# Optimization experiments

Hardware: AMD Instinct MI355X
Metric: run time of the kernel (lower is better)

## Reference

```python
import jax, jax.numpy as jnp
import numpy as np

B, S, D, H = 4, 2048, 1024, 16
HD = D // H

def setup_inputs() -> dict:
    key = jax.random.key(0)
    ks = jax.random.split(key, 5)
    x = jax.random.normal(ks[0], (B, S, D), dtype=jnp.float32)
    mask = jnp.ones((B, S), dtype=jnp.int32)
    # torch nn.Linear init scale ~ 1/sqrt(fan_in); use small normal for stability
    qkv_w = jax.random.normal(ks[1], (3 * D, D), dtype=jnp.float32) * (1.0 / np.sqrt(D))
    qkv_b = jax.random.normal(ks[2], (3 * D,), dtype=jnp.float32) * 0.02
    out_w = jax.random.normal(ks[3], (D, D), dtype=jnp.float32) * (1.0 / np.sqrt(D))
    out_b = jax.random.normal(ks[4], (D,), dtype=jnp.float32) * 0.02
    return {"x": x, "mask": mask, "qkv_w": qkv_w, "qkv_b": qkv_b,
            "out_w": out_w, "out_b": out_b}

def reference(x, mask, qkv_w, qkv_b, out_w, out_b):
    b, s, d = x.shape
    scale = np.sqrt(HD).astype(np.float32)
    # qkv projection: torch Linear y = x @ W^T + b
    qkv = x @ qkv_w.T + qkv_b                      # (b, s, 3d)
    qkv = qkv.reshape(b, s, 3, H, HD)
    qkv = jnp.transpose(qkv, (2, 0, 3, 1, 4))      # (3, b, H, s, hd)
    q, k, v = qkv[0], qkv[1], qkv[2]
    scores = jnp.einsum('bhqd,bhkd->bhqk', q, k) / scale  # (b, H, s, s)
    neg_inf = jnp.float32(-jnp.inf)
    causal = jnp.tril(jnp.ones((s, s), dtype=bool))
    scores = jnp.where(causal[None, None], scores, neg_inf)
    key_mask = (mask != 0)[:, None, None, :]       # (b, 1, 1, s)
    scores = jnp.where(key_mask, scores, neg_inf)
    attn = jax.nn.softmax(scores, axis=-1)
    out = jnp.einsum('bhqk,bhkd->bhqd', attn, v)   # (b, H, s, hd)
    out = jnp.transpose(out, (0, 2, 1, 3)).reshape(b, s, d)
    return out @ out_w.T + out_b
```

## Files before the change

kernel.cpp:

```cpp
#include <hip/hip_runtime.h>
#include <stdint.h>
#include <type_traits>

#define BB  4
#define SS  2048
#define DD  1024
#define HH  16
#define HDD 64

typedef __attribute__((ext_vector_type(8))) short s16x8;
typedef __attribute__((ext_vector_type(4))) float f32x4;

__device__ inline short f2bf(float f) {
    union { float f; unsigned int u; } v; v.f = f;
    unsigned int r = (v.u + 0x7fffu + ((v.u >> 16) & 1u)) >> 16;
    return (short)r;
}

#define GLL(gp, lp) __builtin_amdgcn_global_load_lds( \
    (const __attribute__((address_space(1))) void*)(gp), \
    (__attribute__((address_space(3))) void*)(lp), 16, 0, 0)

#define BAR() asm volatile("s_waitcnt lgkmcnt(0)\n\ts_barrier" ::: "memory")

__global__ void cvt_kernel(const float* __restrict__ src, short* __restrict__ dst, int n) {
    int i = (blockIdx.x * 256 + threadIdx.x) * 8;
    if (i >= n) return;
    const float4* s = (const float4*)(src + i);
    float4 a = s[0], b = s[1];
    s16x8 o;
    o[0]=f2bf(a.x); o[1]=f2bf(a.y); o[2]=f2bf(a.z); o[3]=f2bf(a.w);
    o[4]=f2bf(b.x); o[5]=f2bf(b.y); o[6]=f2bf(b.z); o[7]=f2bf(b.w);
    *(s16x8*)(dst + i) = o;
}

template<int EPI>
__global__ __launch_bounds__(256)
void gemm_bt(const short* __restrict__ A, const short* __restrict__ Bw,
             const float* __restrict__ bias, float* __restrict__ Cf,
             short* __restrict__ Qo, short* __restrict__ Ko, short* __restrict__ Vo,
             int M, int N, int K)
{
    __shared__ short lsA[128 * 32];
    __shared__ short lsB[128 * 32];
    const int tid  = threadIdx.x;
    const int w    = tid >> 6, lane = tid & 63;
    const int quad = lane >> 4, l15 = lane & 15;
    const int m0 = blockIdx.x * 128, n0 = blockIdx.y * 128;
    const int mw = (w & 1) * 64, nw = (w >> 1) * 64;

    f32x4 acc[4][4] = {};

    const int srow = w * 32 + (lane >> 2);
    const int scol = (lane & 3) * 8;
    const short* pA = A + (size_t)(m0 + srow) * K + scol;
    const short* pB = Bw + (size_t)(n0 + srow) * K + scol;
    short* lAbase0 = &lsA[(w * 32) * 32];
    short* lAbase1 = &lsA[(w * 32 + 16) * 32];
    short* lBbase0 = &lsB[(w * 32) * 32];
    short* lBbase1 = &lsB[(w * 32 + 16) * 32];

    for (int kk = 0; kk < K; kk += 32) {
        __syncthreads();
        GLL(pA + kk,            lAbase0);
        GLL(pA + kk + 16 * K,   lAbase1);
        GLL(pB + kk,            lBbase0);
        GLL(pB + kk + 16 * K,   lBbase1);
        asm volatile("s_waitcnt vmcnt(0)" ::: "memory");
        __syncthreads();

        s16x8 af[4], bfr[4];
        for (int t = 0; t < 4; ++t) {
            af[t]  = *(const s16x8*)&lsA[(mw + t * 16 + l15) * 32 + quad * 8];
            bfr[t] = *(const s16x8*)&lsB[(nw + t * 16 + l15) * 32 + quad * 8];
        }
        for (int i = 0; i < 4; ++i)
            for (int j = 0; j < 4; ++j)
                acc[i][j] = __builtin_amdgcn_mfma_f32_16x16x32_bf16(af[i], bfr[j], acc[i][j], 0, 0, 0);
    }

    if (EPI == 0) {
        for (int i = 0; i < 4; ++i) {
            int row = m0 + mw + i * 16 + quad * 4;
            for (int j = 0; j < 4; ++j) {
                int col = n0 + nw + j * 16 + l15;
                float bv = bias[col];
                for (int r = 0; r < 4; ++r)
                    Cf[(size_t)(row + r) * N + col] = acc[i][j][r] + bv;
            }
        }
    } else {
        for (int i = 0; i < 4; ++i) {
            int row = m0 + mw + i * 16 + quad * 4;
            for (int j = 0; j < 4; ++j) {
                int col = n0 + nw + j * 16 + l15;
                float bv = bias[col];
                int sel = col >> 10, h = (col >> 6) & 15, hd = col & 63;
                for (int r = 0; r < 4; ++r) {
                    int rr = row + r;
                    int b = rr >> 11, s = rr & 2047;
                    short val = f2bf(acc[i][j][r] + bv);
                    if (sel == 0)      Qo[(((size_t)b * HH + h) * SS + s) * HDD + hd] = val;
                    else if (sel == 1) Ko[(((size_t)b * HH + h) * SS + s) * HDD + hd] = val;
                    else               Vo[(((size_t)b * HH + h) * HDD + hd) * SS + s] = val;
                }
            }
        }
    }
}

__global__ __launch_bounds__(256, 4)
void attn_kernel(const short* __restrict__ Q, const short* __restrict__ Kb,
                 const short* __restrict__ Vb, const int* __restrict__ mask,
                 short* __restrict__ O)
{
    __shared__ short lsK[128 * 72];
    __shared__ short lsV[64 * 136];
    __shared__ float lsM[128];

    const int tid  = threadIdx.x;
    const int w    = tid >> 6, lane = tid & 63;
    const int quad = lane >> 4, l15 = lane & 15;
    const int bx = blockIdx.x, bh = blockIdx.y;
    const int b = bh >> 4;
    const size_t baseQK = (size_t)bh * SS * HDD;
    const size_t baseV  = (size_t)bh * HDD * SS;
    short* lsPw = &lsK[w * 16 * 136];
    const float SC = 0.18033688f;

    int krow[4], kcs[4], vrow[4], vcs[4];
    for (int i = 0; i < 4; ++i) {
        int ch = tid + i * 256;
        krow[i] = ch >> 3; kcs[i] = (ch & 7) * 8;
        vrow[i] = ch >> 4; vcs[i] = (ch & 15) * 8;
    }

    for (int t = 0; t < 2; ++t) {
        const int qb = t ? bx : (31 - bx);
        const int q0 = qb * 64;
        const int qrow = q0 + w * 16 + l15;
        const int rowg0 = q0 + w * 16 + quad * 4;
        const int T = (qb >> 1) + 1;

        s16x8 aq[2];
        for (int ks = 0; ks < 2; ++ks)
            aq[ks] = *(const s16x8*)(Q + baseQK + (size_t)qrow * HDD + ks * 32 + quad * 8);

        float lsum[4] = {0.f, 0.f, 0.f, 0.f};
        f32x4 o_acc[4] = {};

        s16x8 kc[4], vc[4]; int mc;
        for (int i = 0; i < 4; ++i) {
            kc[i] = *(const s16x8*)(Kb + baseQK + (size_t)krow[i] * HDD + kcs[i]);
            vc[i] = *(const s16x8*)(Vb + baseV + (size_t)vrow[i] * SS + vcs[i]);
        }
        mc = (tid < 128) ? mask[b * SS + tid] : 1;

        auto tile = [&](auto CC, int kt) {
            constexpr bool CAUS = decltype(CC)::value;
            const int kv0 = kt * 128;
            BAR();
            for (int i = 0; i < 4; ++i) {
                *(s16x8*)&lsK[krow[i] * 72 + kcs[i]]  = kc[i];
                *(s16x8*)&lsV[vrow[i] * 136 + vcs[i]] = vc[i];
            }
            if (tid < 128) lsM[tid] = mc ? 0.f : -1e30f;
            if (kt + 1 < T) {
                const int nk = kv0 + 128;
                for (int i = 0; i < 4; ++i) {
                    kc[i] = *(const s16x8*)(Kb + baseQK + (size_t)(nk + krow[i]) * HDD + kcs[i]);
                    vc[i] = *(const s16x8*)(Vb + baseV + (size_t)vrow[i] * SS + nk + vcs[i]);
                }
                mc = (tid < 128) ? mask[b * SS + nk + tid] : 1;
            }
            BAR();

            unsigned int pk[8][2];
            for (int nt = 0; nt < 8; ++nt) {
                f32x4 s = {};
                for (int ks = 0; ks < 2; ++ks) {
                    s16x8 kf = *(const s16x8*)&lsK[(nt * 16 + l15) * 72 + ks * 32 + quad * 8];
                    s = __builtin_amdgcn_mfma_f32_16x16x32_bf16(aq[ks], kf, s, 0, 0, 0);
                }
                float madd = lsM[nt * 16 + l15];
                int colg = kv0 + nt * 16 + l15;
                float p[4];
                for (int r = 0; r < 4; ++r) {
                    float scv = s[r] * SC + madd;
                    if (CAUS && colg > rowg0 + r) scv = -1e30f;
                    p[r] = __builtin_amdgcn_exp2f(scv);
                    lsum[r] += p[r];
                }
                pk[nt][0] = (unsigned int)(unsigned short)f2bf(p[0])
                          | ((unsigned int)(unsigned short)f2bf(p[1]) << 16);
                pk[nt][1] = (unsigned int)(unsigned short)f2bf(p[2])
                          | ((unsigned int)(unsigned short)f2bf(p[3]) << 16);
            }

            BAR();
            for (int nt = 0; nt < 8; ++nt) {
                int off = nt * 16 + l15;
                lsPw[(quad * 4 + 0) * 136 + off] = (short)(pk[nt][0] & 0xffff);
                lsPw[(quad * 4 + 1) * 136 + off] = (short)(pk[nt][0] >> 16);
                lsPw[(quad * 4 + 2) * 136 + off] = (short)(pk[nt][1] & 0xffff);
                lsPw[(quad * 4 + 3) * 136 + off] = (short)(pk[nt][1] >> 16);
            }
            asm volatile("s_waitcnt lgkmcnt(0)" ::: "memory");

            for (int k2 = 0; k2 < 4; ++k2) {
                s16x8 ap = *(const s16x8*)&lsPw[l15 * 136 + k2 * 32 + quad * 8];
                for (int ht = 0; ht < 4; ++ht) {
                    s16x8 vf = *(const s16x8*)&lsV[(ht * 16 + l15) * 136 + k2 * 32 + quad * 8];
                    o_acc[ht] = __builtin_amdgcn_mfma_f32_16x16x32_bf16(ap, vf, o_acc[ht], 0, 0, 0);
                }
            }
        };

        for (int kt = 0; kt < T - 1; ++kt) tile(std::false_type{}, kt);
        tile(std::true_type{}, T - 1);

        const int hcol = (bh & 15) * HDD;
        for (int r = 0; r < 4; ++r) {
            float rs = lsum[r];
            rs += __shfl_xor(rs, 1);
            rs += __shfl_xor(rs, 2);
            rs += __shfl_xor(rs, 4);
            rs += __shfl_xor(rs, 8);
            float inv = 1.0f / rs;
            int srow = q0 + w * 16 + quad * 4 + r;
            size_t base = ((size_t)b * SS + srow) * DD + hcol;
            for (int ht = 0; ht < 4; ++ht)
                O[base + ht * 16 + l15] = f2bf(o_acc[ht][r] * inv);
        }
    }
}

extern "C" void kernel_launch(void* const* d_in, const int* in_sizes, int n_in,
                              void* d_out, int out_size, void* d_ws, size_t ws_size,
                              hipStream_t stream) {
    const float* x     = (const float*)d_in[0];
    const int*   mask  = (const int*)d_in[1];
    const float* qkv_w = (const float*)d_in[2];
    const float* qkv_b = (const float*)d_in[3];
    const float* out_w = (const float*)d_in[4];
    const float* out_b = (const float*)d_in[5];
    float* out = (float*)d_out;

    const size_t M1 = (size_t)BB * SS;
    short* ws  = (short*)d_ws;
    short* xb  = ws;
    short* qwb = xb  + M1 * DD;
    short* owb = qwb + (size_t)3 * DD * DD;
    short* Qb  = owb + (size_t)DD * DD;
    short* Kb  = Qb  + M1 * DD;
    short* Vb  = Kb  + M1 * DD;
    short* Ob  = Vb  + M1 * DD;

    cvt_kernel<<<(int)(M1 * DD / 8 / 256), 256, 0, stream>>>(x, xb, (int)(M1 * DD));
    cvt_kernel<<<3 * DD * DD / 8 / 256, 256, 0, stream>>>(qkv_w, qwb, 3 * DD * DD);
    cvt_kernel<<<DD * DD / 8 / 256, 256, 0, stream>>>(out_w, owb, DD * DD);

    gemm_bt<1><<<dim3(64, 24), 256, 0, stream>>>(xb, qwb, qkv_b, nullptr,
                                                 Qb, Kb, Vb, 8192, 3072, 1024);
    attn_kernel<<<dim3(16, BB * HH), 256, 0, stream>>>(Qb, Kb, Vb, mask, Ob);
    gemm_bt<0><<<dim3(64, 8), 256, 0, stream>>>(Ob, owb, out_b, out,
                                                nullptr, nullptr, nullptr, 8192, 1024, 1024);
}
```

Before: 327.5 us.

## Restructure attention to 32x32 MFMA with transposed scores and register-shuffled P

Rewrites the attention kernel to compute S^T with 32x32x16 bf16 MFMAs, so each lane owns a query row. The P matrix is passed to the PV MFMA through a cross-half lane shuffle instead of a round trip through LDS. K and V tiles are now loaded straight into LDS with global_load_lds and an XOR swizzle, replacing register prefetch into padded LDS. Query blocks grow to 128 rows and the grid halves, which drops the software prefetch overlap and may cut parallelism.

```diff
diff --git a/kernel.cpp b/kernel.cpp
--- a/kernel.cpp
+++ b/kernel.cpp
@@ -8,20 +8,22 @@
 #define HH  16
 #define HDD 64
 
-typedef __attribute__((ext_vector_type(8))) short s16x8;
-typedef __attribute__((ext_vector_type(4))) float f32x4;
+typedef __attribute__((ext_vector_type(8)))  short s16x8;
+typedef __attribute__((ext_vector_type(4)))  float f32x4;
+typedef __attribute__((ext_vector_type(16))) float f32x16;
 
 __device__ inline short f2bf(float f) {
     union { float f; unsigned int u; } v; v.f = f;
     unsigned int r = (v.u + 0x7fffu + ((v.u >> 16) & 1u)) >> 16;
     return (short)r;
 }
+__device__ inline unsigned int pack2bf(float a, float b) {
+    return (unsigned int)(unsigned short)f2bf(a) | ((unsigned int)(unsigned short)f2bf(b) << 16);
+}
 
 #define GLL(gp, lp) __builtin_amdgcn_global_load_lds( \
     (const __attribute__((address_space(1))) void*)(gp), \
     (__attribute__((address_space(3))) void*)(lp), 16, 0, 0)
-
-#define BAR() asm volatile("s_waitcnt lgkmcnt(0)\n\ts_barrier" ::: "memory")
 
 __global__ void cvt_kernel(const float* __restrict__ src, short* __restrict__ dst, int n) {
     int i = (blockIdx.x * 256 + threadIdx.x) * 8;
@@ -114,104 +116,93 @@
                  const short* __restrict__ Vb, const int* __restrict__ mask,
                  short* __restrict__ O)
 {
-    __shared__ short lsK[128 * 72];
-    __shared__ short lsV[64 * 136];
+    __shared__ short lsK[128 * 64];
+    __shared__ short lsV[64 * 128];
     __shared__ float lsM[128];
 
-    const int tid  = threadIdx.x;
-    const int w    = tid >> 6, lane = tid & 63;
-    const int quad = lane >> 4, l15 = lane & 15;
+    const int tid = threadIdx.x;
+    const int w   = tid >> 6, lane = tid & 63;
+    const int h   = lane >> 5, q = lane & 31;
     const int bx = blockIdx.x, bh = blockIdx.y;
     const int b = bh >> 4;
     const size_t baseQK = (size_t)bh * SS * HDD;
     const size_t baseV  = (size_t)bh * HDD * SS;
-    short* lsPw = &lsK[w * 16 * 136];
     const float SC = 0.18033688f;
 
-    int krow[4], kcs[4], vrow[4], vcs[4];
-    for (int i = 0; i < 4; ++i) {
-        int ch = tid + i * 256;
-        krow[i] = ch >> 3; kcs[i] = (ch & 7) * 8;
-        vrow[i] = ch >> 4; vcs[i] = (ch & 15) * 8;
-    }
-
     for (int t = 0; t < 2; ++t) {
-        const int qb = t ? bx : (31 - bx);
-        const int q0 = qb * 64;
-        const int qrow = q0 + w * 16 + l15;
-        const int rowg0 = q0 + w * 16 + quad * 4;
-        const int T = (qb >> 1) + 1;
-
-        s16x8 aq[2];
-        for (int ks = 0; ks < 2; ++ks)
-            aq[ks] = *(const s16x8*)(Q + baseQK + (size_t)qrow * HDD + ks * 32 + quad * 8);
-
-        float lsum[4] = {0.f, 0.f, 0.f, 0.f};
-        f32x4 o_acc[4] = {};
-
-        s16x8 kc[4], vc[4]; int mc;
-        for (int i = 0; i < 4; ++i) {
-            kc[i] = *(const s16x8*)(Kb + baseQK + (size_t)krow[i] * HDD + kcs[i]);
-            vc[i] = *(const s16x8*)(Vb + baseV + (size_t)vrow[i] * SS + vcs[i]);
-        }
-        mc = (tid < 128) ? mask[b * SS + tid] : 1;
+        const int qb = t ? bx : (15 - bx);
+        const int q0 = qb * 128;
+        const int s_row = q0 + w * 32 + q;
+        const int T = qb + 1;
+
+        s16x8 bq[4];
+        for (int kb = 0; kb < 4; ++kb)
+            bq[kb] = *(const s16x8*)(Q + baseQK + (size_t)s_row * HDD + kb * 16 + h * 8);
+
+        float lsum = 0.f;
+        f32x16 oa[2] = {};
 
         auto tile = [&](auto CC, int kt) {
             constexpr bool CAUS = decltype(CC)::value;
             const int kv0 = kt * 128;
-            BAR();
+            __syncthreads();
             for (int i = 0; i < 4; ++i) {
-                *(s16x8*)&lsK[krow[i] * 72 + kcs[i]]  = kc[i];
-                *(s16x8*)&lsV[vrow[i] * 136 + vcs[i]] = vc[i];
-            }
-            if (tid < 128) lsM[tid] = mc ? 0.f : -1e30f;
-            if (kt + 1 < T) {
-                const int nk = kv0 + 128;
-                for (int i = 0; i < 4; ++i) {
-                    kc[i] = *(const s16x8*)(Kb + baseQK + (size_t)(nk + krow[i]) * HDD + kcs[i]);
-                    vc[i] = *(const s16x8*)(Vb + baseV + (size_t)vrow[i] * SS + nk + vcs[i]);
-                }
-                mc = (tid < 128) ? mask[b * SS + nk + tid] : 1;
-            }
-            BAR();
-
-            unsigned int pk[8][2];
-            for (int nt = 0; nt < 8; ++nt) {
-                f32x4 s = {};
-                for (int ks = 0; ks < 2; ++ks) {
-                    s16x8 kf = *(const s16x8*)&lsK[(nt * 16 + l15) * 72 + ks * 32 + quad * 8];
-                    s = __builtin_amdgcn_mfma_f32_16x16x32_bf16(aq[ks], kf, s, 0, 0, 0);
-                }
-                float madd = lsM[nt * 16 + l15];
-                int colg = kv0 + nt * 16 + l15;
-                float p[4];
-                for (int r = 0; r < 4; ++r) {
-                    float scv = s[r] * SC + madd;
-                    if (CAUS && colg > rowg0 + r) scv = -1e30f;
-                    p[r] = __builtin_amdgcn_exp2f(scv);
-                    lsum[r] += p[r];
-                }
-                pk[nt][0] = (unsigned int)(unsigned short)f2bf(p[0])
-                          | ((unsigned int)(unsigned short)f2bf(p[1]) << 16);
-                pk[nt][1] = (unsigned int)(unsigned short)f2bf(p[2])
-                          | ((unsigned int)(unsigned short)f2bf(p[3]) << 16);
-            }
-
-            BAR();
-            for (int nt = 0; nt < 8; ++nt) {
-                int off = nt * 16 + l15;
-                lsPw[(quad * 4 + 0) * 136 + off] = (short)(pk[nt][0] & 0xffff);
-                lsPw[(quad * 4 + 1) * 136 + off] = (short)(pk[nt][0] >> 16);
-                lsPw[(quad * 4 + 2) * 136 + off] = (short)(pk[nt][1] & 0xffff);
-                lsPw[(quad * 4 + 3) * 136 + off] = (short)(pk[nt][1] >> 16);
-            }
-            asm volatile("s_waitcnt lgkmcnt(0)" ::: "memory");
-
-            for (int k2 = 0; k2 < 4; ++k2) {
-                s16x8 ap = *(const s16x8*)&lsPw[l15 * 136 + k2 * 32 + quad * 8];
-                for (int ht = 0; ht < 4; ++ht) {
-                    s16x8 vf = *(const s16x8*)&lsV[(ht * 16 + l15) * 136 + k2 * 32 + quad * 8];
-                    o_acc[ht] = __builtin_amdgcn_mfma_f32_16x16x32_bf16(ap, vf, o_acc[ht], 0, 0, 0);
+                const int p0 = w * 256 + i * 64;
+                const int p  = p0 + lane;
+                const int key = p >> 3, cck = (p & 7) ^ (key & 7);
+                GLL(Kb + baseQK + (size_t)(kv0 + key) * HDD + cck * 8, &lsK[p0 * 8]);
+                const int hd = p >> 4, ccv = (p & 15) ^ (hd & 15);
+                GLL(Vb + baseV + (size_t)hd * SS + kv0 + ccv * 8, &lsV[p0 * 8]);
+            }
+            if (tid < 32) {
+                int4 mv = *(const int4*)(mask + b * SS + kv0 + tid * 4);
+                float4 f;
+                f.x = mv.x ? 0.f : -1e30f; f.y = mv.y ? 0.f : -1e30f;
+                f.z = mv.z ? 0.f : -1e30f; f.w = mv.w ? 0.f : -1e30f;
+                *(float4*)&lsM[tid * 4] = f;
+            }
+            __syncthreads();
+
+            for (int nt = 0; nt < 4; ++nt) {
+                f32x16 sa = {};
+                for (int kb = 0; kb < 4; ++kb) {
+                    const int key = nt * 32 + q;
+                    const int cc  = (kb * 2 + h) ^ (key & 7);
+                    s16x8 ak = *(const s16x8*)&lsK[(key * 8 + cc) * 8];
+                    sa = __builtin_amdgcn_mfma_f32_32x32x16_bf16(ak, bq[kb], sa, 0, 0, 0);
+                }
+                unsigned int pk2[4][2];
+                for (int g = 0; g < 4; ++g) {
+                    float4 mq = *(const float4*)&lsM[nt * 32 + 8 * g + 4 * h];
+                    float pv[4];
+                    for (int r = 0; r < 4; ++r) {
+                        float v = sa[g * 4 + r] * SC + ((const float*)&mq)[r];
+                        if (CAUS) {
+                            int key_l = nt * 32 + r + 8 * g + 4 * h;
+                            if (key_l > w * 32 + q) v = -1e30f;
+                        }
+                        float p = __builtin_amdgcn_exp2f(v);
+                        pv[r] = p;
+                        lsum += p;
+                    }
+                    pk2[g][0] = pack2bf(pv[0], pv[1]);
+                    pk2[g][1] = pack2bf(pv[2], pv[3]);
+                }
+                for (int kb2 = 0; kb2 < 2; ++kb2) {
+                    const int g_own = 2 * kb2 + h;
+                    unsigned int s0 = h ? pk2[2 * kb2][0] : pk2[2 * kb2 + 1][0];
+                    unsigned int s1 = h ? pk2[2 * kb2][1] : pk2[2 * kb2 + 1][1];
+                    unsigned int r0 = (unsigned int)__shfl_xor((int)s0, 32);
+                    unsigned int r1 = (unsigned int)__shfl_xor((int)s1, 32);
+                    union { s16x8 v; unsigned int d[4]; } bp;
+                    if (h == 0) { bp.d[0] = pk2[g_own][0]; bp.d[1] = pk2[g_own][1]; bp.d[2] = r0; bp.d[3] = r1; }
+                    else        { bp.d[0] = r0; bp.d[1] = r1; bp.d[2] = pk2[g_own][0]; bp.d[3] = pk2[g_own][1]; }
+                    for (int mt = 0; mt < 2; ++mt) {
+                        const int hd = mt * 32 + q;
+                        const int cc = ((nt * 2 + kb2) * 2 + h) ^ (hd & 15);
+                        s16x8 av = *(const s16x8*)&lsV[(hd * 16 + cc) * 8];
+                        oa[mt] = __builtin_amdgcn_mfma_f32_32x32x16_bf16(av, bp.v, oa[mt], 0, 0, 0);
+                    }
                 }
             }
         };
@@ -219,18 +210,18 @@
         for (int kt = 0; kt < T - 1; ++kt) tile(std::false_type{}, kt);
         tile(std::true_type{}, T - 1);
 
+        float ls2 = lsum + __shfl_xor(lsum, 32);
+        float inv = 1.0f / ls2;
         const int hcol = (bh & 15) * HDD;
-        for (int r = 0; r < 4; ++r) {
-            float rs = lsum[r];
-            rs += __shfl_xor(rs, 1);
-            rs += __shfl_xor(rs, 2);
-            rs += __shfl_xor(rs, 4);
-            rs += __shfl_xor(rs, 8);
-            float inv = 1.0f / rs;
-            int srow = q0 + w * 16 + quad * 4 + r;
-            size_t base = ((size_t)b * SS + srow) * DD + hcol;
-            for (int ht = 0; ht < 4; ++ht)
-                O[base + ht * 16 + l15] = f2bf(o_acc[ht][r] * inv);
+        const size_t obase = ((size_t)b * SS + s_row) * DD + hcol;
+        for (int mt = 0; mt < 2; ++mt) {
+            for (int g = 0; g < 4; ++g) {
+                const int hd0 = mt * 32 + 8 * g + 4 * h;
+                unsigned int lo = pack2bf(oa[mt][g * 4 + 0] * inv, oa[mt][g * 4 + 1] * inv);
+                unsigned int hi = pack2bf(oa[mt][g * 4 + 2] * inv, oa[mt][g * 4 + 3] * inv);
+                uint2 st; st.x = lo; st.y = hi;
+                *(uint2*)&O[obase + hd0] = st;
+            }
         }
     }
 }
@@ -262,7 +253,7 @@
 
     gemm_bt<1><<<dim3(64, 24), 256, 0, stream>>>(xb, qwb, qkv_b, nullptr,
                                                  Qb, Kb, Vb, 8192, 3072, 1024);
-    attn_kernel<<<dim3(16, BB * HH), 256, 0, stream>>>(Qb, Kb, Vb, mask, Ob);
+    attn_kernel<<<dim3(8, BB * HH), 256, 0, stream>>>(Qb, Kb, Vb, mask, Ob);
     gemm_bt<0><<<dim3(64, 8), 256, 0, stream>>>(Ob, owb, out_b, out,
                                                 nullptr, nullptr, nullptr, 8192, 1024, 1024);
 }
```

New measurement: 325.0 us. No clear change (-0.8%).
